# Performance work log

Measured on AMD Instinct MI355X. Metric: run time of the kernel, lower is better.

The kernel has to match this reference:

```python
import jax, jax.numpy as jnp
import numpy as np

DIM = 128
N = 4096


def setup_inputs() -> dict:
    key = jax.random.key(0)
    ks = jax.random.split(key, 12)
    d = DIM
    s = 0.02
    inp = jax.random.normal(ks[0], (N, 2 * d), dtype=jnp.float32)
    # H = myLinear: (2d -> 5d -> 1), tanh after each layer
    Hw1 = jax.random.normal(ks[1], (2 * d, 5 * d), dtype=jnp.float32) * s
    Hb1 = jax.random.normal(ks[2], (5 * d,), dtype=jnp.float32) * s
    Hw2 = jax.random.normal(ks[3], (5 * d, 1), dtype=jnp.float32) * s
    Hb2 = jax.random.normal(ks[4], (1,), dtype=jnp.float32) * s
    # augment_f: (d -> 4d -> 8d -> d*d), tanh after each layer
    Aw1 = jax.random.normal(ks[5], (d, 4 * d), dtype=jnp.float32) * s
    Ab1 = jax.random.normal(ks[6], (4 * d,), dtype=jnp.float32) * s
    Aw2 = jax.random.normal(ks[7], (4 * d, 8 * d), dtype=jnp.float32) * s
    Ab2 = jax.random.normal(ks[8], (8 * d,), dtype=jnp.float32) * s
    Aw3 = jax.random.normal(ks[9], (8 * d, d * d), dtype=jnp.float32) * s
    Ab3 = jax.random.normal(ks[10], (d * d,), dtype=jnp.float32) * s
    u = jax.random.uniform(ks[11], (d,), dtype=jnp.float32, minval=-0.001, maxval=0.001)
    return {"t": 0, "inp": inp, "Hw1": Hw1, "Hb1": Hb1, "Hw2": Hw2, "Hb2": Hb2,
            "Aw1": Aw1, "Ab1": Ab1, "Aw2": Aw2, "Ab2": Ab2, "Aw3": Aw3, "Ab3": Ab3, "u": u}


def reference(t, inp, Hw1, Hb1, Hw2, Hb2, Aw1, Ab1, Aw2, Ab2, Aw3, Ab3, u):
    d = DIM
    n = inp.shape[0]

    def H_scalar(z):  # z: [2d] -> scalar
        h = jnp.tanh(z @ Hw1 + Hb1)
        return jnp.tanh(h @ Hw2 + Hb2)[0]

    # per-sample gradient of scalar H w.r.t. input (== batch_jacobian squeeze)
    g = jax.vmap(jax.grad(H_scalar))(inp)  # [N, 2d]
    dx = g[:, :d]
    dv = -g[:, d:]

    x = inp[:, :d]
    h1 = jnp.tanh(x @ Aw1 + Ab1)            # [N, 4d]
    h2 = jnp.tanh(h1 @ Aw2 + Ab2)           # [N, 8d]
    gq = jnp.tanh(h2 @ Aw3 + Ab3).reshape(n, d, d)  # [N, d, d]
    dv = dv + jnp.einsum("nij,j->ni", gq, u)
    return jnp.concatenate([dx, dv], axis=-1)  # [N, 2d]
```

## Files before the change

### kernel.cpp

```cpp
#include <hip/hip_runtime.h>
#include <hip/hip_bf16.h>
#include <cstdint>


typedef __bf16 bf16_t;
typedef __bf16 bf16x4_t __attribute__((ext_vector_type(4)));
typedef __bf16 bf16x8_t __attribute__((ext_vector_type(8)));
typedef float f32x4_t __attribute__((ext_vector_type(4)));
typedef float f32x16_t __attribute__((ext_vector_type(16)));
typedef int intx4_t __attribute__((ext_vector_type(4)));
typedef int intx8_t __attribute__((ext_vector_type(8)));

#define DIMD 128
#define NROW 4096
#define SMEM_G64 24576
#define SMEM3_BYTES 24576

__device__ __forceinline__ float fast_tanh(float x) {
  float t = __builtin_amdgcn_exp2f(x * 2.8853900817779268f);
  return 1.f - 2.f * __builtin_amdgcn_rcpf(t + 1.f);
}

__device__ __forceinline__ uint8_t to_fp8(float x) {
  return (uint8_t)(__builtin_amdgcn_cvt_pk_fp8_f32(x, x, 0, false) & 0xff);
}

__device__ __forceinline__ uint32_t pk4_fp8(float a, float b, float c,
                                            float d) {
  uint32_t lo = (uint32_t)__builtin_amdgcn_cvt_pk_fp8_f32(a, b, 0, false);
  return (uint32_t)__builtin_amdgcn_cvt_pk_fp8_f32(c, d, lo, true);
}

__device__ __forceinline__ void g2l16(const void* gp, void* lp) {
  __builtin_amdgcn_global_load_lds(
      reinterpret_cast<__attribute__((address_space(1))) void*>(
          reinterpret_cast<uintptr_t>(gp)),
      reinterpret_cast<__attribute__((address_space(3))) void*>(
          reinterpret_cast<uintptr_t>(lp)),
      16, 0, 0);
}

template <int CTRL>
__device__ __forceinline__ float dpp_addf(float v) {
  return v + __int_as_float(__builtin_amdgcn_update_dpp(
                 0, __float_as_int(v), CTRL, 0xf, 0xf, true));
}
__device__ __forceinline__ float dpp_sum32(float v) {
  v = dpp_addf<0x111>(v);
  v = dpp_addf<0x112>(v);
  v = dpp_addf<0x114>(v);
  v = dpp_addf<0x118>(v);
  v = dpp_addf<0x142>(v);
  return v;
}

template <int EPI>
__device__ __forceinline__ void gemm64_body(char* smem, int bx, int by,
                                            const bf16_t* A, int lda,
                                            const bf16_t* B, int ldb, int K,
                                            const float* bias, void* outp,
                                            int ldo) {
  constexpr int BK = 32;
  bf16_t* As = (bf16_t*)smem;
  bf16_t* Bs = As + 3 * 2048;
  const int NT = K / BK;

  const int m0 = bx * 64;
  const int n0 = by * 64;
  const int tid = threadIdx.x;
  const int wave = tid >> 6;
  const int lane = tid & 63;
  const int wm = wave >> 1;
  const int wn = wave & 1;

  const int sr = lane >> 2;
  const int sk = (((lane & 3) ^ ((sr >> 1) & 3)) * 8);
  const int fr = lane & 15;
  const int fk = (((lane >> 4) ^ ((fr >> 1) & 3)) * 8);
  const int rb = wave * 16;

  const bf16_t* Ag = A + (size_t)(m0 + rb + sr) * lda + sk;
  const bf16_t* Bg = B + (size_t)(n0 + rb + sr) * ldb + sk;

#define G64_STAGE(buf, k0)                              \
  do {                                                  \
    g2l16(Ag + (k0), As + (buf) * 2048 + rb * BK);      \
    g2l16(Bg + (k0), Bs + (buf) * 2048 + rb * BK);      \
  } while (0)

  f32x4_t acc[2][2] = {};

  G64_STAGE(0, 0);
  G64_STAGE(1, BK);
  asm volatile("s_waitcnt vmcnt(2)" ::: "memory");
  __builtin_amdgcn_s_barrier();
  asm volatile("" ::: "memory");

  for (int t = 0; t < NT; ++t) {
    if (t + 2 < NT) G64_STAGE((t + 2) % 3, (t + 2) * BK);
    const bf16_t* Ab = As + (t % 3) * 2048;
    const bf16_t* Bb = Bs + (t % 3) * 2048;

    bf16x8_t af[2], bb[2];
#pragma unroll
    for (int u = 0; u < 2; ++u) {
      af[u] = *(const bf16x8_t*)(Ab + (wm * 32 + u * 16 + fr) * BK + fk);
      bb[u] = *(const bf16x8_t*)(Bb + (wn * 32 + u * 16 + fr) * BK + fk);
    }
#pragma unroll
    for (int i = 0; i < 2; ++i)
#pragma unroll
      for (int j = 0; j < 2; ++j)
        acc[i][j] = __builtin_amdgcn_mfma_f32_16x16x32_bf16(af[i], bb[j],
                                                            acc[i][j], 0, 0, 0);
    if (t < NT - 1) {
      if (t + 2 < NT)
        asm volatile("s_waitcnt vmcnt(2)" ::: "memory");
      else
        asm volatile("s_waitcnt vmcnt(0)" ::: "memory");
      __builtin_amdgcn_s_barrier();
      asm volatile("" ::: "memory");
    }
  }
#undef G64_STAGE

#pragma unroll
  for (int i = 0; i < 2; ++i) {
    const int row = m0 + wm * 32 + i * 16 + (lane >> 4) * 4;
#pragma unroll
    for (int j = 0; j < 2; ++j) {
      const int col = n0 + wn * 32 + j * 16 + fr;
      if constexpr (EPI == 0) {
        bf16_t* O = (bf16_t*)outp;
        const float b = bias[col];
#pragma unroll
        for (int r = 0; r < 4; ++r)
          O[(size_t)(row + r) * ldo + col] = (bf16_t)fast_tanh(acc[i][j][r] + b);
      } else if constexpr (EPI == 1) {
        float* O = (float*)outp;
        const bool dx = (n0 < DIMD);
#pragma unroll
        for (int r = 0; r < 4; ++r) {
          const size_t idx = (size_t)(row + r) * ldo + col;
          if (dx) O[idx] = acc[i][j][r];
          else atomicAdd(&O[idx], -acc[i][j][r]);
        }
      } else {
        uint8_t* O = (uint8_t*)outp;
        const float b = bias[col];
        const int kb = col >> 6;
        const int khalf = (col >> 5) & 1;
        const int kin = col & 31;
#pragma unroll
        for (int r = 0; r < 4; ++r) {
          const int rw = row + r;
          O[(size_t)((rw >> 5) * 16 + kb) * 2048 +
            (khalf * 32 + (rw & 31)) * 32 + kin] =
              to_fp8(64.f * fast_tanh(acc[i][j][r] + b));
        }
      }
    }
  }
}

__device__ __forceinline__ void a3_body(int bx, int by, const uint8_t* AF,
                                        const uint8_t* BF, float* out,
                                        const float* ab3, const float* uvec) {
  const int tid = threadIdx.x;
  const int wave = tid >> 6;
  const int lane = tid & 63;
  const int wm = wave >> 1;
  const int wn = wave & 1;
  const int rl = lane & 31;
  const int m0 = bx * 128;
  const int n0 = by * 128;

  const uint8_t* bp[4];
#pragma unroll
  for (int i = 0; i < 2; ++i)
    bp[i] = AF + (size_t)(bx * 4 + wm * 2 + i) * 16 * 2048 + lane * 32;
#pragma unroll
  for (int j = 0; j < 2; ++j)
    bp[2 + j] = BF + (size_t)(by * 4 + wn * 2 + j) * 16 * 2048 + lane * 32;

  f32x16_t acc[2][2] = {};
  intx8_t s0[4], s1[4], s2[4];

#define A3_LD(S, koff)                                                       \
  _Pragma("unroll") for (int q = 0; q < 4; ++q) {                            \
    *(intx4_t*)&S[q] = *(const intx4_t*)(bp[q] + (koff)*2048);               \
    *((intx4_t*)&S[q] + 1) = *(const intx4_t*)(bp[q] + (koff)*2048 + 16);    \
  }

#define A3_MM(S)                                                             \
  acc[0][0] = __builtin_amdgcn_mfma_scale_f32_32x32x64_f8f6f4(               \
      S[0], S[2], acc[0][0], 0, 0, 0, 0x79797979, 0, 0x79797979);            \
  acc[0][1] = __builtin_amdgcn_mfma_scale_f32_32x32x64_f8f6f4(               \
      S[0], S[3], acc[0][1], 0, 0, 0, 0x79797979, 0, 0x79797979);            \
  acc[1][0] = __builtin_amdgcn_mfma_scale_f32_32x32x64_f8f6f4(               \
      S[1], S[2], acc[1][0], 0, 0, 0, 0x79797979, 0, 0x79797979);            \
  acc[1][1] = __builtin_amdgcn_mfma_scale_f32_32x32x64_f8f6f4(               \
      S[1], S[3], acc[1][1], 0, 0, 0, 0x79797979, 0, 0x79797979);

  A3_LD(s0, 0) A3_LD(s1, 1) A3_LD(s2, 2)
  A3_MM(s0) A3_LD(s0, 3)
  A3_MM(s1) A3_LD(s1, 4)
  A3_MM(s2) A3_LD(s2, 5)
  A3_MM(s0) A3_LD(s0, 6)
  A3_MM(s1) A3_LD(s1, 7)
  A3_MM(s2) A3_LD(s2, 8)
  A3_MM(s0) A3_LD(s0, 9)
  A3_MM(s1) A3_LD(s1, 10)
  A3_MM(s2) A3_LD(s2, 11)
  A3_MM(s0) A3_LD(s0, 12)
  A3_MM(s1) A3_LD(s1, 13)
  A3_MM(s2) A3_LD(s2, 14)
  A3_MM(s0) A3_LD(s0, 15)
  A3_MM(s1)
  A3_MM(s2)
  A3_MM(s0)
#undef A3_LD
#undef A3_MM

  const int q = lane >> 5;
  float uu[2], b3[2];
#pragma unroll
  for (int j = 0; j < 2; ++j) {
    uu[j] = uvec[wn * 64 + j * 32 + rl];
    b3[j] = ab3[n0 + wn * 64 + j * 32 + rl];
  }
  const int ocol = 128 + by;
#pragma unroll
  for (int i = 0; i < 2; ++i) {
    float s16[16];
#pragma unroll
    for (int r = 0; r < 16; ++r)
      s16[r] = fast_tanh(acc[i][0][r] + b3[0]) * uu[0] +
               fast_tanh(acc[i][1][r] + b3[1]) * uu[1];
#pragma unroll
    for (int r = 0; r < 16; ++r) s16[r] = dpp_sum32(s16[r]);
    if (rl == 31) {
      const int rowb = m0 + wm * 64 + i * 32 + 4 * q;
#pragma unroll
      for (int r = 0; r < 16; ++r)
        atomicAdd(&out[(size_t)(rowb + (r & 3) + 8 * (r >> 2)) * 256 + ocol],
                  s16[r]);
    }
  }
}

__device__ __forceinline__ void tcvt_body(char* smem, const float* in,
                                          bf16_t* out, int R, int C, int bx,
                                          int by) {
  float(*t)[33] = (float(*)[33])smem;
  const int c0 = bx * 32;
  const int r0 = by * 32;
  const int tx = threadIdx.x & 31;
  const int ty = threadIdx.x >> 5;
#pragma unroll
  for (int k = 0; k < 4; ++k)
    t[ty + k * 8][tx] = in[(size_t)(r0 + ty + k * 8) * C + c0 + tx];
  __syncthreads();
#pragma unroll
  for (int k = 0; k < 4; ++k)
    out[(size_t)(c0 + ty + k * 8) * R + r0 + tx] = (bf16_t)t[tx][ty + k * 8];
}

__device__ __forceinline__ void aw3t_body(char* smem, const float* Aw3,
                                          uint8_t* Aw3T8F, int b) {
  uint32_t(*T)[33] = (uint32_t(*)[33])smem;
  const int ct = b & 127;
  const int rt = b >> 7;
  const size_t c0 = (size_t)ct * 128;
  const int r0 = rt * 128;
  const int tx = threadIdx.x & 31;
  const int g = threadIdx.x >> 5;
#pragma unroll
  for (int k = 0; k < 4; ++k) {
    const int rr = r0 + 4 * g + 32 * k;
    const float4 v0 = *(const float4*)(Aw3 + (size_t)(rr + 0) * 16384 + c0 + 4 * tx);
    const float4 v1 = *(const float4*)(Aw3 + (size_t)(rr + 1) * 16384 + c0 + 4 * tx);
    const float4 v2 = *(const float4*)(Aw3 + (size_t)(rr + 2) * 16384 + c0 + 4 * tx);
    const float4 v3 = *(const float4*)(Aw3 + (size_t)(rr + 3) * 16384 + c0 + 4 * tx);
    const int r4 = g + 8 * k;
    T[4 * tx + 0][r4] = pk4_fp8(64.f * v0.x, 64.f * v1.x, 64.f * v2.x, 64.f * v3.x);
    T[4 * tx + 1][r4] = pk4_fp8(64.f * v0.y, 64.f * v1.y, 64.f * v2.y, 64.f * v3.y);
    T[4 * tx + 2][r4] = pk4_fp8(64.f * v0.z, 64.f * v1.z, 64.f * v2.z, 64.f * v3.z);
    T[4 * tx + 3][r4] = pk4_fp8(64.f * v0.w, 64.f * v1.w, 64.f * v2.w, 64.f * v3.w);
  }
  __syncthreads();
  const int kb = (rt << 1) + (tx >> 4);
  const int khalf = (tx >> 3) & 1;
  const int kin = (tx & 7) << 2;
#pragma unroll
  for (int k2 = 0; k2 < 16; ++k2) {
    const int cc = g + 8 * k2;
    const int cb = (ct << 2) + (cc >> 5);
    const int cin = cc & 31;
    *(uint32_t*)(Aw3T8F + (size_t)(cb * 16 + kb) * 2048 +
                 (khalf * 32 + cin) * 32 + kin) = T[cc][tx];
  }
}

__device__ __forceinline__ void hgrad_row(int row, const bf16_t* h,
                                          const float* Hw2, const float* Hb2,
                                          bf16_t* wout) {
  const int lane = threadIdx.x & 63;
  float hv[10], wv[10];
  float pre2 = 0.f;
#pragma unroll
  for (int t = 0; t < 10; ++t) {
    const int j = lane + t * 64;
    hv[t] = (float)h[(size_t)row * 640 + j];
    wv[t] = Hw2[j];
    pre2 += hv[t] * wv[t];
  }
#pragma unroll
  for (int d = 1; d < 64; d <<= 1) pre2 += __shfl_xor(pre2, d, 64);
  const float y = fast_tanh(pre2 + Hb2[0]);
  const float s = 1.f - y * y;
#pragma unroll
  for (int t = 0; t < 10; ++t) {
    const int j = lane + t * 64;
    wout[(size_t)row * 640 + j] = (bf16_t)(s * wv[t] * (1.f - hv[t] * hv[t]));
  }
}

__global__ __launch_bounds__(256) void launch0(
    const float* __restrict__ inp, bf16_t* __restrict__ inp_bf,
    const float* __restrict__ Hw1, bf16_t* __restrict__ Hw1T,
    bf16_t* __restrict__ Hw1_bf, const float* __restrict__ Aw1,
    bf16_t* __restrict__ Aw1T, const float* __restrict__ Aw2,
    bf16_t* __restrict__ Aw2T, float* __restrict__ out) {
  __shared__ __align__(16) char smem[4224];
  int b = blockIdx.x;
  if (b < 1024) {
    const int i = b * 256 + threadIdx.x;
    const float4 v = ((const float4*)inp)[i];
    bf16x4_t o = {(bf16_t)v.x, (bf16_t)v.y, (bf16_t)v.z, (bf16_t)v.w};
    ((bf16x4_t*)inp_bf)[i] = o;
  } else if (b < 1184) {
    int s = b - 1024;
    tcvt_body(smem, Hw1, Hw1T, 256, 640, s % 20, s / 20);
  } else if (b < 1248) {
    int s = b - 1184;
    tcvt_body(smem, Aw1, Aw1T, 128, 512, s % 16, s / 16);
  } else if (b < 1760) {
    int s = b - 1248;
    tcvt_body(smem, Aw2, Aw2T, 512, 1024, s % 32, s / 32);
  } else if (b < 1920) {
    const int i = (b - 1760) * 256 + threadIdx.x;
    const float4 v = ((const float4*)Hw1)[i];
    bf16x4_t o = {(bf16_t)v.x, (bf16_t)v.y, (bf16_t)v.z, (bf16_t)v.w};
    ((bf16x4_t*)Hw1_bf)[i] = o;
  } else {
    const int i = (b - 1920) * 256 + threadIdx.x;
    ((float4*)out)[i] = make_float4(0.f, 0.f, 0.f, 0.f);
  }
}

__global__ __launch_bounds__(256) void launch1(
    const bf16_t* __restrict__ inp_bf, const bf16_t* __restrict__ Hw1T,
    const float* __restrict__ Hb1, bf16_t* __restrict__ h_bf,
    const bf16_t* __restrict__ Aw1T, const float* __restrict__ Ab1,
    bf16_t* __restrict__ h1_bf, const float* __restrict__ Aw3,
    uint8_t* __restrict__ Aw3T8F) {
  __shared__ __align__(16) char smem[SMEM_G64];
  const int b = blockIdx.x;
  if (b < 640) {
    gemm64_body<0>(smem, b % 64, b / 64, inp_bf, 256, Hw1T, 256, 256, Hb1,
                   h_bf, 640);
  } else if (b < 1152) {
    const int i = b - 640;
    gemm64_body<0>(smem, i % 64, i / 64, inp_bf, 256, Aw1T, 128, 128, Ab1,
                   h1_bf, 512);
  } else {
    aw3t_body(smem, Aw3, Aw3T8F, b - 1152);
  }
}

__global__ __launch_bounds__(256) void launch2(
    const bf16_t* __restrict__ h1_bf, const bf16_t* __restrict__ Aw2T,
    const float* __restrict__ Ab2, uint8_t* __restrict__ h2F,
    const bf16_t* __restrict__ h_bf, const float* __restrict__ Hw2,
    const float* __restrict__ Hb2, bf16_t* __restrict__ w_bf,
    const float* __restrict__ Aw3, uint8_t* __restrict__ Aw3T8F) {
  __shared__ __align__(16) char smem[SMEM_G64];
  const int b = blockIdx.x;
  if (b < 1024) {
    gemm64_body<4>(smem, b % 64, b / 64, h1_bf, 512, Aw2T, 512, 512, Ab2,
                   h2F, 0);
  } else if (b < 2048) {
    const int row = (b - 1024) * 4 + (threadIdx.x >> 6);
    hgrad_row(row, h_bf, Hw2, Hb2, w_bf);
  } else {
    aw3t_body(smem, Aw3, Aw3T8F, 512 + (b - 2048));
  }
}

__global__ __launch_bounds__(256, 3) void launch3(
    const bf16_t* __restrict__ w_bf, const bf16_t* __restrict__ Hw1_bf,
    float* __restrict__ out, const uint8_t* __restrict__ h2F,
    const uint8_t* __restrict__ Aw3T8F, const float* __restrict__ Ab3,
    const float* __restrict__ uvec) {
  __shared__ __align__(16) char smem[SMEM3_BYTES];
  const int b = blockIdx.x;
  if (b < 256) {
    gemm64_body<1>(smem, b % 64, b / 64, w_bf, 640, Hw1_bf, 640, 640, nullptr,
                   out, 256);
  } else {
    const int p = b - 256;
    const int by = (p & 7) * 16 + ((p >> 3) & 15);
    const int bx = p >> 7;
    a3_body(bx, by, h2F, Aw3T8F, out, Ab3, uvec);
  }
}

extern "C" void kernel_launch(void* const* d_in, const int* in_sizes, int n_in,
                              void* d_out, int out_size, void* d_ws,
                              size_t ws_size, hipStream_t stream) {
  (void)in_sizes; (void)n_in; (void)out_size; (void)ws_size;
  const float* inp = (const float*)d_in[1];
  const float* Hw1 = (const float*)d_in[2];
  const float* Hb1 = (const float*)d_in[3];
  const float* Hw2 = (const float*)d_in[4];
  const float* Hb2 = (const float*)d_in[5];
  const float* Aw1 = (const float*)d_in[6];
  const float* Ab1 = (const float*)d_in[7];
  const float* Aw2 = (const float*)d_in[8];
  const float* Ab2 = (const float*)d_in[9];
  const float* Aw3 = (const float*)d_in[10];
  const float* Ab3 = (const float*)d_in[11];
  const float* u = (const float*)d_in[12];
  float* out = (float*)d_out;

  char* ws = (char*)d_ws;
  bf16_t* inp_bf = (bf16_t*)ws;    ws += (size_t)NROW * 256 * 2;
  bf16_t* Hw1_bf = (bf16_t*)ws;    ws += (size_t)256 * 640 * 2;
  bf16_t* Hw1T = (bf16_t*)ws;      ws += (size_t)640 * 256 * 2;
  bf16_t* Aw1T = (bf16_t*)ws;      ws += (size_t)512 * 128 * 2;
  bf16_t* Aw2T = (bf16_t*)ws;      ws += (size_t)1024 * 512 * 2;
  uint8_t* Aw3T8F = (uint8_t*)ws;  ws += (size_t)16384 * 1024;
  bf16_t* h_bf = (bf16_t*)ws;      ws += (size_t)NROW * 640 * 2;
  bf16_t* w_bf = (bf16_t*)ws;      ws += (size_t)NROW * 640 * 2;
  bf16_t* h1_bf = (bf16_t*)ws;     ws += (size_t)NROW * 512 * 2;
  uint8_t* h2F = (uint8_t*)ws;     ws += (size_t)NROW * 1024;

  launch0<<<2944, 256, 0, stream>>>(inp, inp_bf, Hw1, Hw1T, Hw1_bf, Aw1, Aw1T,
                                    Aw2, Aw2T, out);
  launch1<<<1664, 256, 0, stream>>>(inp_bf, Hw1T, Hb1, h_bf, Aw1T, Ab1, h1_bf,
                                    Aw3, Aw3T8F);
  launch2<<<2560, 256, 0, stream>>>(h1_bf, Aw2T, Ab2, h2F, h_bf, Hw2, Hb2,
                                    w_bf, Aw3, Aw3T8F);
  launch3<<<4352, 256, 0, stream>>>(w_bf, Hw1_bf, out, h2F, Aw3T8F, Ab3, u);
}
```

Measured before the change: 240.6 us.

## Stage fp8 A tiles through LDS with triple-buffered async loads in a3 GEMM

The h2 fp8 activations are now written row-major rather than in a pre-swizzled MFMA fragment layout. The big Aw3 GEMM stages A tiles into shared memory with direct global-to-LDS copies. It uses a three-deep ring buffer, XOR swizzling and barriers per k-step, while B fragments are still loaded directly into registers with double buffering. The goal is to share A loads across the waves of a block, so each wave stops re-fetching its own fragment copy from global memory. The cost is LDS traffic, per-iteration barriers and hand-tuned vmcnt waits that could stall or be miscounted.

```diff
diff --git a/kernel.cpp b/kernel.cpp
--- a/kernel.cpp
+++ b/kernel.cpp
@@ -148,79 +148,98 @@
       } else {
         uint8_t* O = (uint8_t*)outp;
         const float b = bias[col];
-        const int kb = col >> 6;
-        const int khalf = (col >> 5) & 1;
-        const int kin = col & 31;
-#pragma unroll
-        for (int r = 0; r < 4; ++r) {
-          const int rw = row + r;
-          O[(size_t)((rw >> 5) * 16 + kb) * 2048 +
-            (khalf * 32 + (rw & 31)) * 32 + kin] =
+#pragma unroll
+        for (int r = 0; r < 4; ++r)
+          O[(size_t)(row + r) * ldo + col] =
               to_fp8(64.f * fast_tanh(acc[i][j][r] + b));
-        }
       }
     }
   }
 }
 
-__device__ __forceinline__ void a3_body(int bx, int by, const uint8_t* AF,
+__device__ __forceinline__ void a3_body(char* smem, int bx, int by,
+                                        const uint8_t* Arow,
                                         const uint8_t* BF, float* out,
                                         const float* ab3, const float* uvec) {
+  constexpr int NT = 16;
+  uint8_t* As = (uint8_t*)smem;
+
   const int tid = threadIdx.x;
   const int wave = tid >> 6;
   const int lane = tid & 63;
   const int wm = wave >> 1;
   const int wn = wave & 1;
   const int rl = lane & 31;
+  const int c0 = lane >> 5;
   const int m0 = bx * 128;
   const int n0 = by * 128;
 
-  const uint8_t* bp[4];
-#pragma unroll
-  for (int i = 0; i < 2; ++i)
-    bp[i] = AF + (size_t)(bx * 4 + wm * 2 + i) * 16 * 2048 + lane * 32;
-#pragma unroll
-  for (int j = 0; j < 2; ++j)
-    bp[2 + j] = BF + (size_t)(by * 4 + wn * 2 + j) * 16 * 2048 + lane * 32;
+  const int sr = lane >> 2;
+  const int sk = ((lane & 3) ^ ((sr >> 1) & 3)) * 16;
+  const uint8_t* Ag = Arow + (size_t)(m0 + wave * 32 + sr) * 1024 + sk;
+  const int lbase = wave * 2048;
+
+#define A3_STAGE(buf, k0)                                                \
+  do {                                                                   \
+    g2l16(Ag + (size_t)(k0) * 64, As + (buf) * 8192 + lbase);            \
+    g2l16(Ag + 16 * 1024 + (size_t)(k0) * 64,                            \
+          As + (buf) * 8192 + lbase + 1024);                             \
+  } while (0)
+
+  const uint8_t* Bg0 = BF + (size_t)(by * 4 + wn * 2 + 0) * 16 * 2048 + lane * 32;
+  const uint8_t* Bg1 = BF + (size_t)(by * 4 + wn * 2 + 1) * 16 * 2048 + lane * 32;
 
   f32x16_t acc[2][2] = {};
-  intx8_t s0[4], s1[4], s2[4];
-
-#define A3_LD(S, koff)                                                       \
-  _Pragma("unroll") for (int q = 0; q < 4; ++q) {                            \
-    *(intx4_t*)&S[q] = *(const intx4_t*)(bp[q] + (koff)*2048);               \
-    *((intx4_t*)&S[q] + 1) = *(const intx4_t*)(bp[q] + (koff)*2048 + 16);    \
-  }
-
-#define A3_MM(S)                                                             \
-  acc[0][0] = __builtin_amdgcn_mfma_scale_f32_32x32x64_f8f6f4(               \
-      S[0], S[2], acc[0][0], 0, 0, 0, 0x79797979, 0, 0x79797979);            \
-  acc[0][1] = __builtin_amdgcn_mfma_scale_f32_32x32x64_f8f6f4(               \
-      S[0], S[3], acc[0][1], 0, 0, 0, 0x79797979, 0, 0x79797979);            \
-  acc[1][0] = __builtin_amdgcn_mfma_scale_f32_32x32x64_f8f6f4(               \
-      S[1], S[2], acc[1][0], 0, 0, 0, 0x79797979, 0, 0x79797979);            \
-  acc[1][1] = __builtin_amdgcn_mfma_scale_f32_32x32x64_f8f6f4(               \
-      S[1], S[3], acc[1][1], 0, 0, 0, 0x79797979, 0, 0x79797979);
-
-  A3_LD(s0, 0) A3_LD(s1, 1) A3_LD(s2, 2)
-  A3_MM(s0) A3_LD(s0, 3)
-  A3_MM(s1) A3_LD(s1, 4)
-  A3_MM(s2) A3_LD(s2, 5)
-  A3_MM(s0) A3_LD(s0, 6)
-  A3_MM(s1) A3_LD(s1, 7)
-  A3_MM(s2) A3_LD(s2, 8)
-  A3_MM(s0) A3_LD(s0, 9)
-  A3_MM(s1) A3_LD(s1, 10)
-  A3_MM(s2) A3_LD(s2, 11)
-  A3_MM(s0) A3_LD(s0, 12)
-  A3_MM(s1) A3_LD(s1, 13)
-  A3_MM(s2) A3_LD(s2, 14)
-  A3_MM(s0) A3_LD(s0, 15)
-  A3_MM(s1)
-  A3_MM(s2)
-  A3_MM(s0)
-#undef A3_LD
-#undef A3_MM
+  intx8_t bb[2][2];
+
+#define B_LOAD(par, t)                                                    \
+  do {                                                                    \
+    *(intx4_t*)&bb[par][0] = *(const intx4_t*)(Bg0 + (size_t)(t) * 2048); \
+    *((intx4_t*)&bb[par][0] + 1) =                                        \
+        *(const intx4_t*)(Bg0 + (size_t)(t) * 2048 + 16);                 \
+    *(intx4_t*)&bb[par][1] = *(const intx4_t*)(Bg1 + (size_t)(t) * 2048); \
+    *((intx4_t*)&bb[par][1] + 1) =                                        \
+        *(const intx4_t*)(Bg1 + (size_t)(t) * 2048 + 16);                 \
+  } while (0)
+
+  A3_STAGE(0, 0);
+  A3_STAGE(1, 1);
+  B_LOAD(0, 0);
+  asm volatile("s_waitcnt vmcnt(6)" ::: "memory");
+  __builtin_amdgcn_s_barrier();
+  asm volatile("" ::: "memory");
+
+  const int w = (rl >> 1) & 3;
+  const int sLo = ((2 * c0) ^ w) * 16;
+  const int sHi = ((2 * c0 + 1) ^ w) * 16;
+
+#pragma unroll
+  for (int t = 0; t < NT; ++t) {
+    if (t + 2 < NT) A3_STAGE((t + 2) % 3, t + 2);
+    if (t + 1 < NT) B_LOAD((t + 1) & 1, t + 1);
+    const uint8_t* Ab = As + (t % 3) * 8192;
+#pragma unroll
+    for (int i = 0; i < 2; ++i) {
+      const int ra = (wm * 64 + i * 32 + rl) * 64;
+      intx8_t af;
+      *(intx4_t*)&af = *(const intx4_t*)(Ab + ra + sLo);
+      *((intx4_t*)&af + 1) = *(const intx4_t*)(Ab + ra + sHi);
+#pragma unroll
+      for (int j = 0; j < 2; ++j)
+        acc[i][j] = __builtin_amdgcn_mfma_scale_f32_32x32x64_f8f6f4(
+            af, bb[t & 1][j], acc[i][j], 0, 0, 0, 0x79797979, 0, 0x79797979);
+    }
+    if (t < NT - 1) {
+      if (t + 2 < NT)
+        asm volatile("s_waitcnt vmcnt(6)" ::: "memory");
+      else
+        asm volatile("s_waitcnt vmcnt(4)" ::: "memory");
+      __builtin_amdgcn_s_barrier();
+      asm volatile("" ::: "memory");
+    }
+  }
+#undef A3_STAGE
+#undef B_LOAD
 
   const int q = lane >> 5;
   float uu[2], b3[2];
@@ -381,15 +400,15 @@
 
 __global__ __launch_bounds__(256) void launch2(
     const bf16_t* __restrict__ h1_bf, const bf16_t* __restrict__ Aw2T,
-    const float* __restrict__ Ab2, uint8_t* __restrict__ h2F,
+    const float* __restrict__ Ab2, uint8_t* __restrict__ h2_f8,
     const bf16_t* __restrict__ h_bf, const float* __restrict__ Hw2,
     const float* __restrict__ Hb2, bf16_t* __restrict__ w_bf,
     const float* __restrict__ Aw3, uint8_t* __restrict__ Aw3T8F) {
   __shared__ __align__(16) char smem[SMEM_G64];
   const int b = blockIdx.x;
   if (b < 1024) {
-    gemm64_body<4>(smem, b % 64, b / 64, h1_bf, 512, Aw2T, 512, 512, Ab2,
-                   h2F, 0);
+    gemm64_body<3>(smem, b % 64, b / 64, h1_bf, 512, Aw2T, 512, 512, Ab2,
+                   h2_f8, 1024);
   } else if (b < 2048) {
     const int row = (b - 1024) * 4 + (threadIdx.x >> 6);
     hgrad_row(row, h_bf, Hw2, Hb2, w_bf);
@@ -400,7 +419,7 @@
 
 __global__ __launch_bounds__(256, 3) void launch3(
     const bf16_t* __restrict__ w_bf, const bf16_t* __restrict__ Hw1_bf,
-    float* __restrict__ out, const uint8_t* __restrict__ h2F,
+    float* __restrict__ out, const uint8_t* __restrict__ h2_f8,
     const uint8_t* __restrict__ Aw3T8F, const float* __restrict__ Ab3,
     const float* __restrict__ uvec) {
   __shared__ __align__(16) char smem[SMEM3_BYTES];
@@ -412,7 +431,7 @@
     const int p = b - 256;
     const int by = (p & 7) * 16 + ((p >> 3) & 15);
     const int bx = p >> 7;
-    a3_body(bx, by, h2F, Aw3T8F, out, Ab3, uvec);
+    a3_body(smem, bx, by, h2_f8, Aw3T8F, out, Ab3, uvec);
   }
 }
 
@@ -444,13 +463,13 @@
   bf16_t* h_bf = (bf16_t*)ws;      ws += (size_t)NROW * 640 * 2;
   bf16_t* w_bf = (bf16_t*)ws;      ws += (size_t)NROW * 640 * 2;
   bf16_t* h1_bf = (bf16_t*)ws;     ws += (size_t)NROW * 512 * 2;
-  uint8_t* h2F = (uint8_t*)ws;     ws += (size_t)NROW * 1024;
+  uint8_t* h2_f8 = (uint8_t*)ws;   ws += (size_t)NROW * 1024;
 
   launch0<<<2944, 256, 0, stream>>>(inp, inp_bf, Hw1, Hw1T, Hw1_bf, Aw1, Aw1T,
                                     Aw2, Aw2T, out);
   launch1<<<1664, 256, 0, stream>>>(inp_bf, Hw1T, Hb1, h_bf, Aw1T, Ab1, h1_bf,
                                     Aw3, Aw3T8F);
-  launch2<<<2560, 256, 0, stream>>>(h1_bf, Aw2T, Ab2, h2F, h_bf, Hw2, Hb2,
+  launch2<<<2560, 256, 0, stream>>>(h1_bf, Aw2T, Ab2, h2_f8, h_bf, Hw2, Hb2,
                                     w_bf, Aw3, Aw3T8F);
-  launch3<<<4352, 256, 0, stream>>>(w_bf, Hw1_bf, out, h2F, Aw3T8F, Ab3, u);
-}
+  launch3<<<4352, 256, 0, stream>>>(w_bf, Hw1_bf, out, h2_f8, Aw3T8F, Ab3, u);
+}
```

Result: faster. 232.7 us (-3.3%).
